# Kernel optimization log

Hardware: AMD Instinct MI355X
Metric: run time of the kernel (lower is better)

Reference implementation:

```python
import jax, jax.numpy as jnp
from jax import lax
import numpy as np

# 8-neighbor topology from the original module
TOPO = np.array([[0, 1], [1, 1], [1, 0], [1, -1], [0, -1], [-1, -1], [-1, 0], [-1, 1]])
EPS = 1e-5


def conv(x, w, stride=1, pad=0, groups=1):
    # NCHW / OIHW convolution, no bias (module uses bias=False everywhere)
    return lax.conv_general_dilated(
        x, w, (stride, stride), [(pad, pad), (pad, pad)],
        feature_group_count=groups,
        dimension_numbers=('NCHW', 'OIHW', 'NCHW'))


def bn(x, g, b):
    # training-mode BatchNorm2d (batch statistics, biased variance)
    m = jnp.mean(x, axis=(0, 2, 3), keepdims=True)
    v = jnp.var(x, axis=(0, 2, 3), keepdims=True)
    return g[None, :, None, None] * (x - m) * lax.rsqrt(v + EPS) + b[None, :, None, None]


def setup_inputs() -> dict:
    key = jax.random.key(0)
    ks = jax.random.split(key, 12)
    B, D, NC, H, W = 8, 6, 48, 256, 256
    s = 0.1
    w = lambda k, shape: jax.random.normal(k, shape, jnp.float32) * s
    return dict(
        x=jax.random.normal(ks[0], (B, D, H, W), jnp.float32),
        # compenv_conv: Conv(D->NC,1) BN tanh Conv(NC->1,1)
        ce_w1=w(ks[1], (NC, D, 1, 1)), ce_g=jnp.ones(NC), ce_b=jnp.zeros(NC),
        ce_w2=w(ks[2], (1, NC, 1, 1)),
        # merge_change_determinant: funnel(ConvT(10->NC,3) tanh Conv(NC->NC,3) tanh) BN tanh Conv(NC->1,2,s2) sigmoid
        # ConvT stride-1 k3 expressed as pad-2 conv with conv-equivalent kernel
        md_ct=w(ks[3], (NC, 10, 3, 3)), md_c1=w(ks[4], (NC, NC, 3, 3)),
        md_g=jnp.ones(NC), md_b=jnp.zeros(NC), md_c2=w(ks[5], (1, NC, 2, 2)),
        # cell_merge: Conv(D->NC,2,s2,g3) BN tanh funnel(ConvT(NC->NC,3,g3) tanh Conv(NC->D,3,g3) tanh)
        cm_w1=w(ks[6], (NC, D // 3, 2, 2)), cm_g=jnp.ones(NC), cm_b=jnp.zeros(NC),
        cm_ct=w(ks[7], (NC, NC // 3, 3, 3)), cm_c2=w(ks[8], (D, NC // 3, 3, 3)),
        # born: Conv(D->NC,1) BN tanh Conv(NC->D,1)
        bo_w1=w(ks[9], (NC, D, 1, 1)), bo_g=jnp.ones(NC), bo_b=jnp.zeros(NC),
        bo_w2=w(ks[10], (D, NC, 1, 1)),
    )


def reference(x, ce_w1, ce_g, ce_b, ce_w2, md_ct, md_c1, md_g, md_b, md_c2,
              cm_w1, cm_g, cm_b, cm_ct, cm_c2, bo_w1, bo_g, bo_b, bo_w2):
    # ---- compenv: per-direction roll + 1x1conv/BN/tanh/1x1conv (BN stats per direction, as in torch) ----
    env = []
    for k in range(8):
        t = jnp.roll(x, int(TOPO[k, 0]), axis=3)      # roll_right along W
        t = jnp.roll(t, int(-TOPO[k, 1]), axis=2)     # roll_down along H
        h = jnp.tanh(bn(conv(t, ce_w1), ce_g, ce_b))
        env.append(conv(h, ce_w2))                    # [B,1,H,W]
    ENV = jnp.concatenate(env, axis=1)                # [B,8,H,W]

    # ---- merge change determinant ----
    te = jnp.concatenate([x[:, :2], ENV], axis=1)     # [B,10,H,W]
    h = jnp.tanh(conv(te, md_ct, pad=2))              # ConvT k3 s1 == pad-2 conv -> [B,NC,H+2,W+2]
    h = jnp.tanh(conv(h, md_c1))                      # -> [B,NC,H,W]
    h = jnp.tanh(bn(h, md_g, md_b))
    CHANGE = jax.nn.sigmoid(conv(h, md_c2, stride=2))  # [B,1,H/2,W/2]

    # ---- cell merge ----
    h = jnp.tanh(bn(conv(x, cm_w1, stride=2, groups=3), cm_g, cm_b))  # [B,NC,H/2,W/2]
    h = jnp.tanh(conv(h, cm_ct, pad=2, groups=3))
    xm = jnp.tanh(conv(h, cm_c2, groups=3))           # [B,D,H/2,W/2]

    # ---- born + blend ----
    born = conv(jnp.tanh(bn(conv(xm, bo_w1), bo_g, bo_b)), bo_w2)
    out = xm * (1.0 - CHANGE) + CHANGE * born
    out = jnp.concatenate([jax.nn.sigmoid(out[:, :3]), out[:, 3:]], axis=1)
    return out
```

## Files before the change

kernel.cpp:

```cpp
#include <hip/hip_runtime.h>
#include <stdint.h>

typedef unsigned short ushort_t;

#define B8  8
#define D6  6
#define NC  48
#define HH  256
#define WW  256
#define HWp 65536
#define H2  128
#define HW2 16384

__device__ __constant__ int c_T0[8] = {0,1,1,1,0,-1,-1,-1};
__device__ __constant__ int c_T1[8] = {1,1,0,-1,-1,-1,0,1};

__device__ inline float bf2f(ushort_t u){ union{unsigned int i; float f;} w; w.i = ((unsigned int)u)<<16; return w.f; }
__device__ inline ushort_t f2bf(float f){ union{float f; unsigned int i;} w; w.f=f; unsigned int xx=w.i;
  return (ushort_t)((xx + 0x7fffu + ((xx>>16)&1u)) >> 16); }
__device__ inline float tanhf_(float x){ float e=__expf(2.f*x); return 1.f - 2.f/(e+1.f); }
__device__ inline float sigm_(float x){ return 1.f/(1.f+__expf(-x)); }
__device__ inline float ldg_(const void* p, size_t i, int isbf){
  return isbf ? bf2f(((const ushort_t*)p)[i]) : ((const float*)p)[i];
}

typedef short short8 __attribute__((ext_vector_type(8)));
typedef float f4 __attribute__((ext_vector_type(4)));
typedef ushort_t us4 __attribute__((ext_vector_type(4)));
typedef ushort_t us8 __attribute__((ext_vector_type(8)));
union AB { short8 s; us4 h[2]; us8 u; };

__device__ inline void msb_inline(int c, const float* mom, const float* W1,
      const void* g, const void* b, int isbf, float invN, float* sc, float* bi){
  const int st[6]={0,6,11,15,18,20};
  float wr[6];
  #pragma unroll
  for(int d=0;d<6;d++) wr[d]=W1[c*6+d];
  float mean=0.f;
  #pragma unroll
  for(int d=0;d<6;d++) mean += wr[d]*mom[d];
  mean *= invN;
  float e2=0.f;
  #pragma unroll
  for(int d=0;d<6;d++)
    #pragma unroll
    for(int e=d;e<6;e++)
      e2 += wr[d]*wr[e]*((e==d)?1.f:2.f)*mom[6 + st[d] + (e-d)];
  e2 *= invN;
  float var = e2 - mean*mean;
  float s = ldg_(g,c,isbf) * rsqrtf(var + 1e-5f);
  sc[c]=s; bi[c]= ldg_(b,c,isbf) - s*mean;
}

__device__ inline void csb_inline(int c, const float* stats, const void* g, const void* b,
      int isbf, float invN, float* sc, float* bi){
  float mean=stats[2*c]*invN; float var=stats[2*c+1]*invN - mean*mean;
  float s=ldg_(g,c,isbf)*rsqrtf(var+1e-5f);
  sc[c]=s; bi[c]=ldg_(b,c,isbf)-s*mean;
}

__global__ __launch_bounds__(256) void k_detect(const ushort_t* x, float* stats){
  int t=threadIdx.x;
  for(int i=t;i<1024;i+=256) stats[i]=0.f;
  __syncthreads();
  int cnt=0;
  for(int i=t;i<4096;i+=256){
    ushort_t u=x[2*i];
    int e=(u>>7)&0xff;
    if(e>=100 && e<=150) cnt++;
  }
  for(int o=32;o;o>>=1) cnt+=__shfl_down(cnt,o,64);
  __shared__ int sh4[4];
  if((t&63)==0) sh4[t>>6]=cnt;
  __syncthreads();
  if(t==0){ int tot=sh4[0]+sh4[1]+sh4[2]+sh4[3]; stats[960] = (tot>=2048)?1.f:0.f; }
}

struct WC { const ushort_t* src[10]; int off[10]; int n[10]; };

__global__ __launch_bounds__(256) void k_prep(WC wc, float* dst, const float* dfl,
      const void* mdc1r, const void* mdctr, ushort_t* wb2, ushort_t* wb1,
      const void* x, float* xmom){
  int isbf = dfl[0]>0.5f;
  int bx = blockIdx.x;
  __shared__ float red[4][27];
  if(bx < 810){
    int arr = bx/81, blk = bx-arr*81;
    int n = wc.n[arr]; const ushort_t* s = wc.src[arr]; float* d = dst + wc.off[arr];
    for(int i = blk*256 + threadIdx.x; i < n; i += 81*256)
      d[i] = isbf ? bf2f(s[i]) : ((const float*)s)[i];
  } else if(bx < 831){
    int t = (bx-810)*256+threadIdx.x;
    if(t<3456){
      int lane=t&63; int rest=t>>6;
      int ks=rest&1; int g=rest>>1; int tap=g%9; int nt=g/9;
      int oc=nt*16+(lane&15); int icb=ks*32+((lane>>4)*8);
      #pragma unroll
      for(int j=0;j<8;j++){
        int ic=icb+j;
        float v = (ic<48) ? ldg_(mdc1r,(size_t)(oc*48+ic)*9+tap,isbf) : 0.f;
        wb2[(size_t)t*8+j]=f2bf(v);
      }
    } else if(t<5184){
      int tt=t-3456; int lane=tt&63; int g=tt>>6; int tap=g%9; int nt=g/9;
      int oc=nt*16+(lane&15); int icb=(lane>>4)*8;
      #pragma unroll
      for(int j=0;j<8;j++){
        int ic=icb+j;
        float v = (ic<10) ? ldg_(mdctr,(size_t)(oc*10+ic)*9+tap,isbf) : 0.f;
        wb1[(size_t)tt*8+j]=f2bf(v);
      }
    }
  } else {
    int bm = bx-831;
    float vals[27];
    #pragma unroll
    for(int i=0;i<27;i++) vals[i]=0.f;
    for(int p = bm*256+threadIdx.x; p < B8*HWp; p += 256*256){
      int b = p >> 16; int hw = p & 65535;
      float v[6];
      #pragma unroll
      for(int d=0; d<6; d++) v[d]=ldg_(x, (((size_t)(b*6+d))<<16)+hw, isbf);
      int q=6;
      #pragma unroll
      for(int d=0;d<6;d++){
        vals[d]+=v[d];
        #pragma unroll
        for(int e=d;e<6;e++){ vals[q] += v[d]*v[e]; q++; }
      }
    }
    int wid=threadIdx.x>>6, lane=threadIdx.x&63;
    #pragma unroll
    for(int i=0;i<27;i++){
      float v=vals[i];
      for(int o=32;o;o>>=1) v+=__shfl_down(v,o,64);
      if(lane==0) red[wid][i]=v;
    }
    __syncthreads();
    if(threadIdx.x<27)
      atomicAdd(&xmom[threadIdx.x],
        red[0][threadIdx.x]+red[1][threadIdx.x]+red[2][threadIdx.x]+red[3][threadIdx.x]);
  }
}

__global__ __launch_bounds__(256) void k_envcm1(const void* x, const float* dfl,
      const float* xmom, const float* cew1, const float* cew2, const void* ceg, const void* ceb,
      const float* cmw1, float* e, ushort_t* t1){
  int isbf = dfl[0]>0.5f;
  int bx = blockIdx.x;
  __shared__ float sc[48], bi[48];
  if(bx < 2048){
    if(threadIdx.x<48)
      msb_inline(threadIdx.x, xmom, cew1, ceg, ceb, isbf, 1.f/(float)(B8*HWp), sc, bi);
    __syncthreads();
    int p = bx*256+threadIdx.x;
    int b = p >> 16; int hw = p & 65535;
    float v[6];
    #pragma unroll
    for(int d=0; d<6; d++) v[d]=ldg_(x,(size_t)(b*6+d)*HWp + hw, isbf);
    float acc=0.f;
    for(int c=0;c<NC;c++){
      float y=0.f;
      #pragma unroll
      for(int d=0;d<6;d++) y += cew1[c*6+d]*v[d];
      acc += cew2[c]*tanhf_(sc[c]*y + bi[c]);
    }
    e[(size_t)b*HWp + hw]=acc;
  } else {
    int p=(bx-2048)*256+threadIdx.x;
    int b=p>>14; int rem=p&16383; int i=rem>>7; int j=rem&127;
    float v[6][2][2];
    #pragma unroll
    for(int d=0;d<6;d++)
      #pragma unroll
      for(int ki=0;ki<2;ki++)
        #pragma unroll
        for(int kj=0;kj<2;kj++)
          v[d][ki][kj]=ldg_(x, ((size_t)(b*6+d)*HH + 2*i+ki)*WW + 2*j+kj, isbf);
    for(int oc=0;oc<NC;oc++){
      int g=oc>>4;
      float a=0.f;
      #pragma unroll
      for(int icl=0;icl<2;icl++)
        #pragma unroll
        for(int ki=0;ki<2;ki++)
          #pragma unroll
          for(int kj=0;kj<2;kj++)
            a += v[2*g+icl][ki][kj]*cmw1[((oc*2+icl)*2+ki)*2+kj];
      t1[((size_t)(b*NC+oc)*HW2) + rem]=f2bf(a);
    }
  }
}

__global__ __launch_bounds__(256,3) void k_mdst(const void* x, const float* dfl, const float* e,
      const ushort_t* wb1, const ushort_t* wb2, ushort_t* h2t, float* stats,
      const ushort_t* t1, float* t1stats){
  __shared__ __attribute__((aligned(16))) ushort_t te[6400];
  __shared__ __attribute__((aligned(16))) ushort_t h1t[19488];
  __shared__ float red[4][3][16][2];
  int bx = blockIdx.x;
  if(bx >= 2048){
    int l = bx-2048;
    int c = l % NC; int s = l / NC;
    float sum=0.f, sq=0.f;
    for(int b=0;b<B8;b++){
      size_t base=((size_t)b*NC+c)*HW2;
      for(int i=s*256+threadIdx.x; i<HW2; i+=8*256){
        float v = bf2f(t1[base+i]);
        sum+=v; sq+=v*v;
      }
    }
    for(int o=32;o;o>>=1){ sum+=__shfl_down(sum,o,64); sq+=__shfl_down(sq,o,64); }
    int wid=threadIdx.x>>6;
    if((threadIdx.x&63)==0){ red[wid][0][0][0]=sum; red[wid][0][0][1]=sq; }
    __syncthreads();
    if(threadIdx.x==0){
      atomicAdd(&t1stats[2*c],   red[0][0][0][0]+red[1][0][0][0]+red[2][0][0][0]+red[3][0][0][0]);
      atomicAdd(&t1stats[2*c+1], red[0][0][0][1]+red[1][0][0][1]+red[2][0][0][1]+red[3][0][0][1]);
    }
    return;
  }
  int isbf = dfl[0]>0.5f;
  int b = bx>>8; int tile = bx&255;
  int ti = tile>>4, tj = tile&15;
  int i0 = ti*16, j0 = tj*16;
  int lane = threadIdx.x&63, w = threadIdx.x>>6;
  int n = lane&15, quad = lane>>4;
  {
    us8 z;
    #pragma unroll
    for(int j=0;j<8;j++) z[j]=0;
    us8* tp=(us8*)te;
    for(int idx=threadIdx.x; idx<800; idx+=256) tp[idx]=z;
    for(int idx=threadIdx.x; idx<336; idx+=256) *(us8*)&h1t[idx*58+48]=z;
  }
  __syncthreads();
  for(int idx=threadIdx.x; idx<4000; idx+=256){
    int pix = idx/10, ic = idx-pix*10;
    int r = pix/20, c = pix-r*20;
    int gy = i0-2+r, gx = j0-2+c;
    float v = 0.f;
    if(gy>=0 && gy<HH && gx>=0 && gx<WW){
      if(ic<2) v = ldg_(x, ((size_t)(b*6+ic)*HH + gy)*WW + gx, isbf);
      else { int k=ic-2;
        int yy=(gy + c_T1[k]) & 255; int xx=(gx - c_T0[k]) & 255;
        v = e[((size_t)b*HH + yy)*WW + xx]; }
    }
    te[pix*16+ic]=f2bf(v);
  }
  __syncthreads();
  {
    int qoff = (quad&1)*8;
    for(int mt=w; mt<21; mt+=4){
      int p = mt*16 + n;
      int pr = p/18, pc = p-pr*18;
      f4 hacc[3];
      #pragma unroll
      for(int nt=0;nt<3;nt++) hacc[nt]=(f4){0.f,0.f,0.f,0.f};
      #pragma unroll
      for(int tap=0; tap<9; tap++){
        int ki=tap/3, kj=tap%3;
        AB a; a.u = *(const us8*)&te[((pr+ki)*20 + pc+kj)*16 + qoff];
        #pragma unroll
        for(int nt=0;nt<3;nt++){
          AB Bf; Bf.u = *(const us8*)&wb1[((size_t)((nt*9+tap)*64+lane))*8];
          hacc[nt] = __builtin_amdgcn_mfma_f32_16x16x32_bf16(a.s, Bf.s, hacc[nt], 0,0,0);
        }
      }
      int pd = mt*16 + quad*4;
      #pragma unroll
      for(int nt=0;nt<3;nt++){
        #pragma unroll
        for(int r=0;r<4;r++)
          h1t[(pd+r)*58 + nt*16 + n] = f2bf(tanhf_(hacc[nt][r]));
      }
    }
  }
  __syncthreads();
  f4 acc[4][3];
  #pragma unroll
  for(int a=0;a<4;a++)
    #pragma unroll
    for(int c=0;c<3;c++) acc[a][c]=(f4){0.f,0.f,0.f,0.f};
  int q1off = 32 + ((quad<2) ? quad*8 : 16);
  #pragma unroll
  for(int tap=0; tap<9; tap++){
    int ki=tap/3, kj=tap%3;
    AB Bf[3][2];
    #pragma unroll
    for(int nt=0;nt<3;nt++)
      #pragma unroll
      for(int ks=0;ks<2;ks++)
        Bf[nt][ks].u = *(const us8*)&wb2[((size_t)(((nt*9+tap)*2+ks)*64+lane))*8];
    #pragma unroll
    for(int yy=0; yy<4; yy++){
      int y = w*4 + yy;
      int base = ((y+ki)*18 + n + kj)*58;
      AB a0, a1;
      a0.u = *(const us8*)&h1t[base + quad*8];
      a1.u = *(const us8*)&h1t[base + q1off];
      #pragma unroll
      for(int nt=0;nt<3;nt++){
        acc[yy][nt] = __builtin_amdgcn_mfma_f32_16x16x32_bf16(a0.s, Bf[nt][0].s, acc[yy][nt], 0,0,0);
        acc[yy][nt] = __builtin_amdgcn_mfma_f32_16x16x32_bf16(a1.s, Bf[nt][1].s, acc[yy][nt], 0,0,0);
      }
    }
  }
  float s[3]={0.f,0.f,0.f}, q[3]={0.f,0.f,0.f};
  size_t tilebase = (size_t)bx*48*256;
  #pragma unroll
  for(int yy=0;yy<4;yy++){
    #pragma unroll
    for(int nt=0;nt<3;nt++){
      int oc = nt*16 + n;
      size_t base = tilebase + (size_t)oc*256 + (w*4+yy)*16 + quad*4;
      us4 u;
      #pragma unroll
      for(int r=0;r<4;r++){
        float v=tanhf_(acc[yy][nt][r]);
        u[r]=f2bf(v);
        float vb=bf2f(u[r]);
        s[nt]+=vb; q[nt]+=vb*vb;
      }
      *(us4*)&h2t[base] = u;
    }
  }
  #pragma unroll
  for(int nt=0;nt<3;nt++){
    s[nt]+=__shfl_xor(s[nt],16,64); s[nt]+=__shfl_xor(s[nt],32,64);
    q[nt]+=__shfl_xor(q[nt],16,64); q[nt]+=__shfl_xor(q[nt],32,64);
  }
  if(quad==0){
    #pragma unroll
    for(int nt=0;nt<3;nt++){ red[w][nt][n][0]=s[nt]; red[w][nt][n][1]=q[nt]; }
  }
  __syncthreads();
  if(threadIdx.x<48){
    int oc=threadIdx.x; int nt=oc>>4, nn=oc&15;
    float S=red[0][nt][nn][0]+red[1][nt][nn][0]+red[2][nt][nn][0]+red[3][nt][nn][0];
    float Q=red[0][nt][nn][1]+red[1][nt][nn][1]+red[2][nt][nn][1]+red[3][nt][nn][1];
    atomicAdd(&stats[2*oc],S); atomicAdd(&stats[2*oc+1],Q);
  }
}

__global__ __launch_bounds__(256) void k_chcm2(const ushort_t* h2t, const float* dfl,
      const float* mdstats, const void* mdg, const void* mdb, const float* wc2, float* CH,
      const ushort_t* t1, const float* t1stats, const void* cmg, const void* cmb,
      const float* wct, float* t2){
  __shared__ float shbuf[6816];
  int isbf = dfl[0]>0.5f;
  int bx = blockIdx.x;
  if(bx < 2048){
    float* rr = shbuf; float* sc = shbuf+256; float* bi = shbuf+304;
    if(threadIdx.x<48)
      csb_inline(threadIdx.x, mdstats, mdg, mdb, isbf, 1.f/(float)(B8*HWp), sc, bi);
    __syncthreads();
    int tile = bx;
    int b = tile>>8; int rest = tile&255; int ti = rest>>4, tj = rest&15;
    int t = threadIdx.x;
    int pix = t&63, icq = t>>6;
    int oi = pix>>3, oj = pix&7;
    const ushort_t* tp = &h2t[(size_t)tile*48*256];
    float acc = 0.f;
    #pragma unroll
    for(int icl=0; icl<12; icl++){
      int ic = icq*12 + icl;
      float s = sc[ic], tb = bi[ic];
      const ushort_t* cp = tp + ic*256 + (2*oi)*16 + 2*oj;
      acc += tanhf_(s*bf2f(cp[0 ])+tb)*wc2[ic*4+0];
      acc += tanhf_(s*bf2f(cp[1 ])+tb)*wc2[ic*4+1];
      acc += tanhf_(s*bf2f(cp[16])+tb)*wc2[ic*4+2];
      acc += tanhf_(s*bf2f(cp[17])+tb)*wc2[ic*4+3];
    }
    rr[icq*64+pix] = acc;
    __syncthreads();
    if(t<64){
      float v = rr[t]+rr[64+t]+rr[128+t]+rr[192+t];
      int i = ti*8 + (t>>3), j = tj*8 + (t&7);
      CH[((size_t)b<<14) + i*128 + j] = sigm_(v);
    }
  } else {
    float* as = shbuf; float* sc = shbuf+6720; float* bi = shbuf+6768;
    if(threadIdx.x<48)
      csb_inline(threadIdx.x, t1stats, cmg, cmb, isbf, 1.f/(float)(B8*HW2), sc, bi);
    __syncthreads();
    int l = bx-2048;
    int g = l/648; int rem = l-g*648; int b = rem/81; int t = rem-b*81;
    int ti=t/9, tj=t%9;
    int i0=ti*16, j0=tj*16;
    int ty=threadIdx.x>>4, tx=threadIdx.x&15;
    for(int idx=threadIdx.x; idx<6400; idx+=256){
      int i=idx/400; int rm=idx-i*400; int r=rm/20; int cc=rm-r*20;
      int cg=g*16+i;
      int y=i0-2+r, xx=j0-2+cc;
      float v=0.f;
      if(y>=0 && y<H2 && xx>=0 && xx<H2)
        v = tanhf_(sc[cg]*bf2f(t1[((size_t)(b*NC+cg)*H2 + y)*H2 + xx]) + bi[cg]);
      as[(i*20+r)*21+cc]=v;
    }
    __syncthreads();
    float acc[16];
    #pragma unroll
    for(int o=0;o<16;o++) acc[o]=0.f;
    for(int i=0;i<16;i++){
      float p[3][3];
      #pragma unroll
      for(int ki=0;ki<3;ki++)
        #pragma unroll
        for(int kj=0;kj<3;kj++) p[ki][kj]=as[(i*20+ty+ki)*21+tx+kj];
      #pragma unroll
      for(int o=0;o<16;o++){
        const float* wp=&wct[((size_t)(g*16+o)*16+i)*9];
        float a=0.f;
        #pragma unroll
        for(int q=0;q<9;q++) a += p[q/3][q%3]*wp[q];
        acc[o]+=a;
      }
    }
    int ii=i0+ty, jj=j0+tx;
    if(ii<130 && jj<130){
      #pragma unroll
      for(int o=0;o<16;o++)
        t2[((size_t)(b*NC+g*16+o)*130 + ii)*130 + jj]=tanhf_(acc[o]);
    }
  }
}

__global__ __launch_bounds__(256) void k_cm3(const float* t2, const float* w, float* xm){
  __shared__ float ts[16][18][20];
  int b=blockIdx.y, g=blockIdx.z;
  int ti=blockIdx.x>>3, tj=blockIdx.x&7;
  int i0=ti*16, j0=tj*16;
  int ty=threadIdx.x>>4, tx=threadIdx.x&15;
  for(int idx=threadIdx.x; idx<16*18*18; idx+=256){
    int i=idx/324; int rem=idx-i*324; int r=rem/18; int cc=rem-r*18;
    int cg=g*16+i;
    ts[i][r][cc]=t2[((size_t)(b*NC+cg)*130 + i0+r)*130 + j0+cc];
  }
  __syncthreads();
  float acc[2]={0.f,0.f};
  for(int icl=0;icl<16;icl++){
    float p[3][3];
    #pragma unroll
    for(int ki=0;ki<3;ki++)
      #pragma unroll
      for(int kj=0;kj<3;kj++) p[ki][kj]=ts[icl][ty+ki][tx+kj];
    #pragma unroll
    for(int ol=0;ol<2;ol++){
      int oc=2*g+ol;
      const float* wp=&w[((size_t)oc*16+icl)*9];
      float a=0.f;
      #pragma unroll
      for(int q=0;q<9;q++) a += p[q/3][q%3]*wp[q];
      acc[ol]+=a;
    }
  }
  int ii=i0+ty, jj=j0+tx;
  #pragma unroll
  for(int ol=0;ol<2;ol++)
    xm[((size_t)(b*6+2*g+ol)*H2 + ii)*H2 + jj]=tanhf_(acc[ol]);
}

__global__ __launch_bounds__(256) void k_mom(const float* src, float* out){
  float vals[27];
  #pragma unroll
  for(int i=0;i<27;i++) vals[i]=0.f;
  int stride = gridDim.x*256;
  for(int p = blockIdx.x*256+threadIdx.x; p < B8*HW2; p += stride){
    int b = p >> 14; int hw = p & 16383;
    float v[6];
    #pragma unroll
    for(int d=0; d<6; d++) v[d]=src[(((size_t)(b*6+d))<<14)+hw];
    int q=6;
    #pragma unroll
    for(int d=0;d<6;d++){
      vals[d]+=v[d];
      #pragma unroll
      for(int e=d;e<6;e++){ vals[q] += v[d]*v[e]; q++; }
    }
  }
  __shared__ float red[4][27];
  int wid=threadIdx.x>>6, lane=threadIdx.x&63;
  #pragma unroll
  for(int i=0;i<27;i++){
    float v=vals[i];
    for(int o=32;o;o>>=1) v+=__shfl_down(v,o,64);
    if(lane==0) red[wid][i]=v;
  }
  __syncthreads();
  if(threadIdx.x<27)
    atomicAdd(&out[threadIdx.x],
      red[0][threadIdx.x]+red[1][threadIdx.x]+red[2][threadIdx.x]+red[3][threadIdx.x]);
}

__global__ __launch_bounds__(256) void k_final(const float* xm, const float* CH,
      const float* xmmom, const float* w1, const float* w2, const void* bog, const void* bob,
      const float* dfl, void* outp){
  int isbf = dfl[0]>0.5f;
  __shared__ float sc[48], bi[48];
  if(threadIdx.x<48)
    msb_inline(threadIdx.x, xmmom, w1, bog, bob, isbf, 1.f/(float)(B8*HW2), sc, bi);
  __syncthreads();
  int p=blockIdx.x*256+threadIdx.x;
  int b=p>>14; int rem=p&16383;
  float v[6];
  #pragma unroll
  for(int d=0;d<6;d++) v[d]=xm[((size_t)(b*6+d)*HW2)+rem];
  float born[6]={0.f,0.f,0.f,0.f,0.f,0.f};
  for(int c=0;c<NC;c++){
    float y=0.f;
    #pragma unroll
    for(int d=0;d<6;d++) y+=w1[c*6+d]*v[d];
    float a=tanhf_(sc[c]*y+bi[c]);
    #pragma unroll
    for(int d=0;d<6;d++) born[d]+=w2[d*NC+c]*a;
  }
  float C=CH[p];
  #pragma unroll
  for(int d=0;d<6;d++){
    float o=v[d]*(1.f-C)+C*born[d];
    if(d<3) o=sigm_(o);
    size_t id=((size_t)(b*6+d)*HW2)+rem;
    if(isbf) ((ushort_t*)outp)[id]=f2bf(o); else ((float*)outp)[id]=o;
  }
}

extern "C" void kernel_launch(void* const* d_in, const int* in_sizes, int n_in,
                              void* d_out, int out_size, void* d_ws, size_t ws_size,
                              hipStream_t stream){
  (void)in_sizes; (void)n_in; (void)out_size; (void)ws_size;
  const ushort_t* x    = (const ushort_t*)d_in[0];
  const ushort_t* cew1 = (const ushort_t*)d_in[1];
  const void*     ceg  = d_in[2];
  const void*     ceb  = d_in[3];
  const ushort_t* cew2 = (const ushort_t*)d_in[4];
  const ushort_t* mdct = (const ushort_t*)d_in[5];
  const ushort_t* mdc1 = (const ushort_t*)d_in[6];
  const void*     mdg  = d_in[7];
  const void*     mdb  = d_in[8];
  const ushort_t* mdc2 = (const ushort_t*)d_in[9];
  const ushort_t* cmw1 = (const ushort_t*)d_in[10];
  const void*     cmg  = d_in[11];
  const void*     cmb  = d_in[12];
  const ushort_t* cmct = (const ushort_t*)d_in[13];
  const ushort_t* cmc2 = (const ushort_t*)d_in[14];
  const ushort_t* bow1 = (const ushort_t*)d_in[15];
  const void*     bog  = d_in[16];
  const void*     bob  = d_in[17];
  const ushort_t* bow2 = (const ushort_t*)d_in[18];
  float* ws = (float*)d_ws;

  const long OW_mdct=0, OW_mdc1=4320, OW_cew1=25056, OW_cew2=25344, OW_mdc2=25392,
             OW_cmw1=25584, OW_cmct=25968, OW_cmc2=32880, OW_bow1=33744, OW_bow2=34032;
  const long OFF_STATS=34320;
  const long ST_xmom=OFF_STATS+0,
             ST_h2  =OFF_STATS+160,
             ST_t1  =OFF_STATS+352,
             ST_xmm =OFF_STATS+544;
  const long OFF_WB2 = OFF_STATS + 1024;
  const long OFF_WB1 = OFF_WB2 + 13824;
  const long OFF_E   = OFF_WB1 + 6912;
  const long OFF_H2  = OFF_E + 524288L;
  const long OFF_D   = OFF_H2 + 12582912L;
  const long OFF_T1=OFF_D, OFF_T2=OFF_D+6291456L, OFF_XM=OFF_D+12781056L, OFF_CH=OFF_D+13567488L;

  ushort_t* h2t  = (ushort_t*)(ws + OFF_H2);
  ushort_t* t1h  = (ushort_t*)(ws + OFF_T1);
  ushort_t* wb2  = (ushort_t*)(ws + OFF_WB2);
  ushort_t* wb1  = (ushort_t*)(ws + OFF_WB1);
  const float* dfl = ws + OFF_STATS + 960;

  hipLaunchKernelGGL(k_detect, dim3(1), 256, 0, stream, x, ws+OFF_STATS);

  WC wc;
  const ushort_t* srcs[10] = {mdct,mdc1,cew1,cew2,mdc2,cmw1,cmct,cmc2,bow1,bow2};
  const int offs[10] = {(int)OW_mdct,(int)OW_mdc1,(int)OW_cew1,(int)OW_cew2,(int)OW_mdc2,
                        (int)OW_cmw1,(int)OW_cmct,(int)OW_cmc2,(int)OW_bow1,(int)OW_bow2};
  const int cnts[10] = {4320,20736,288,48,192,384,6912,864,288,288};
  for(int i=0;i<10;i++){ wc.src[i]=srcs[i]; wc.off[i]=offs[i]; wc.n[i]=cnts[i]; }
  hipLaunchKernelGGL(k_prep, dim3(1087), 256, 0, stream, wc, ws, dfl,
                     (const void*)mdc1, (const void*)mdct, wb2, wb1, (const void*)x, ws+ST_xmom);

  hipLaunchKernelGGL(k_envcm1, dim3(2560), 256, 0, stream, (const void*)x, dfl,
                     ws+ST_xmom, ws+OW_cew1, ws+OW_cew2, ceg, ceb, ws+OW_cmw1,
                     ws+OFF_E, t1h);

  hipLaunchKernelGGL(k_mdst, dim3(2432), 256, 0, stream, (const void*)x, dfl, ws+OFF_E,
                     wb1, wb2, h2t, ws+ST_h2, t1h, ws+ST_t1);

  hipLaunchKernelGGL(k_chcm2, dim3(3992), 256, 0, stream, h2t, dfl,
                     ws+ST_h2, mdg, mdb, ws+OW_mdc2, ws+OFF_CH,
                     t1h, ws+ST_t1, cmg, cmb, ws+OW_cmct, ws+OFF_T2);

  hipLaunchKernelGGL(k_cm3, dim3(64,8,3), 256, 0, stream, ws+OFF_T2, ws+OW_cmc2, ws+OFF_XM);

  hipLaunchKernelGGL(k_mom, dim3(128), 256, 0, stream, ws+OFF_XM, ws+ST_xmm);

  hipLaunchKernelGGL(k_final, dim3(512), 256, 0, stream, ws+OFF_XM, ws+OFF_CH,
                     ws+ST_xmm, ws+OW_bow1, ws+OW_bow2, bog, bob, dfl, d_out);
}
```

Before: 404.4 us.

## Store h2 in NCHW planar layout and keep t2 intermediate in bf16

k_mdst now writes the tanh conv output h2 in plain NCHW layout instead of per-tile blocks. The CHANGE stage becomes one thread per output pixel that loops over all 48 channels and reads 2x2 windows straight from global memory, which drops the shared-memory reduction and cuts its block count from 2048 to 512. Separately, the cell-merge intermediate t2 is stored as bf16 instead of fp32, halving its traffic into k_cm3. The cost is less coalesced strided reads in the CHANGE path and some extra rounding on t2.

```diff
diff --git a/kernel.cpp b/kernel.cpp
--- a/kernel.cpp
+++ b/kernel.cpp
@@ -193,7 +193,7 @@
 }
 
 __global__ __launch_bounds__(256,3) void k_mdst(const void* x, const float* dfl, const float* e,
-      const ushort_t* wb1, const ushort_t* wb2, ushort_t* h2t, float* stats,
+      const ushort_t* wb1, const ushort_t* wb2, ushort_t* h2h, float* stats,
       const ushort_t* t1, float* t1stats){
   __shared__ __attribute__((aligned(16))) ushort_t te[6400];
   __shared__ __attribute__((aligned(16))) ushort_t h1t[19488];
@@ -307,13 +307,13 @@
     }
   }
   float s[3]={0.f,0.f,0.f}, q[3]={0.f,0.f,0.f};
-  size_t tilebase = (size_t)bx*48*256;
   #pragma unroll
   for(int yy=0;yy<4;yy++){
+    int Y = i0 + w*4 + yy;
     #pragma unroll
     for(int nt=0;nt<3;nt++){
       int oc = nt*16 + n;
-      size_t base = tilebase + (size_t)oc*256 + (w*4+yy)*16 + quad*4;
+      size_t base = ((size_t)(b*NC+oc)*HH + Y)*WW + j0 + quad*4;
       us4 u;
       #pragma unroll
       for(int r=0;r<4;r++){
@@ -322,7 +322,7 @@
         float vb=bf2f(u[r]);
         s[nt]+=vb; q[nt]+=vb*vb;
       }
-      *(us4*)&h2t[base] = u;
+      *(us4*)&h2h[base] = u;
     }
   }
   #pragma unroll
@@ -343,48 +343,37 @@
   }
 }
 
-__global__ __launch_bounds__(256) void k_chcm2(const ushort_t* h2t, const float* dfl,
+__global__ __launch_bounds__(256) void k_chcm2(const ushort_t* h2h, const float* dfl,
       const float* mdstats, const void* mdg, const void* mdb, const float* wc2, float* CH,
       const ushort_t* t1, const float* t1stats, const void* cmg, const void* cmb,
-      const float* wct, float* t2){
+      const float* wct, ushort_t* t2){
   __shared__ float shbuf[6816];
   int isbf = dfl[0]>0.5f;
   int bx = blockIdx.x;
-  if(bx < 2048){
-    float* rr = shbuf; float* sc = shbuf+256; float* bi = shbuf+304;
+  if(bx < 512){
+    float* sc = shbuf; float* bi = shbuf+48;
     if(threadIdx.x<48)
       csb_inline(threadIdx.x, mdstats, mdg, mdb, isbf, 1.f/(float)(B8*HWp), sc, bi);
     __syncthreads();
-    int tile = bx;
-    int b = tile>>8; int rest = tile&255; int ti = rest>>4, tj = rest&15;
-    int t = threadIdx.x;
-    int pix = t&63, icq = t>>6;
-    int oi = pix>>3, oj = pix&7;
-    const ushort_t* tp = &h2t[(size_t)tile*48*256];
-    float acc = 0.f;
-    #pragma unroll
-    for(int icl=0; icl<12; icl++){
-      int ic = icq*12 + icl;
-      float s = sc[ic], tb = bi[ic];
-      const ushort_t* cp = tp + ic*256 + (2*oi)*16 + 2*oj;
-      acc += tanhf_(s*bf2f(cp[0 ])+tb)*wc2[ic*4+0];
-      acc += tanhf_(s*bf2f(cp[1 ])+tb)*wc2[ic*4+1];
-      acc += tanhf_(s*bf2f(cp[16])+tb)*wc2[ic*4+2];
-      acc += tanhf_(s*bf2f(cp[17])+tb)*wc2[ic*4+3];
-    }
-    rr[icq*64+pix] = acc;
-    __syncthreads();
-    if(t<64){
-      float v = rr[t]+rr[64+t]+rr[128+t]+rr[192+t];
-      int i = ti*8 + (t>>3), j = tj*8 + (t&7);
-      CH[((size_t)b<<14) + i*128 + j] = sigm_(v);
-    }
+    int p=bx*256+threadIdx.x;
+    int b=p>>14; int rem=p&16383; int i=rem>>7; int j=rem&127;
+    float acc=0.f;
+    for(int ic=0;ic<NC;ic++){
+      size_t base=((size_t)(b*NC+ic)*HH + 2*i)*WW + 2*j;
+      float s=sc[ic], t=bi[ic];
+      #pragma unroll
+      for(int ki=0;ki<2;ki++)
+        #pragma unroll
+        for(int kj=0;kj<2;kj++)
+          acc += tanhf_(s*bf2f(h2h[base+(size_t)ki*WW+kj])+t)*wc2[ic*4+ki*2+kj];
+    }
+    CH[p]=sigm_(acc);
   } else {
     float* as = shbuf; float* sc = shbuf+6720; float* bi = shbuf+6768;
     if(threadIdx.x<48)
       csb_inline(threadIdx.x, t1stats, cmg, cmb, isbf, 1.f/(float)(B8*HW2), sc, bi);
     __syncthreads();
-    int l = bx-2048;
+    int l = bx-512;
     int g = l/648; int rem = l-g*648; int b = rem/81; int t = rem-b*81;
     int ti=t/9, tj=t%9;
     int i0=ti*16, j0=tj*16;
@@ -421,12 +410,12 @@
     if(ii<130 && jj<130){
       #pragma unroll
       for(int o=0;o<16;o++)
-        t2[((size_t)(b*NC+g*16+o)*130 + ii)*130 + jj]=tanhf_(acc[o]);
-    }
-  }
-}
-
-__global__ __launch_bounds__(256) void k_cm3(const float* t2, const float* w, float* xm){
+        t2[((size_t)(b*NC+g*16+o)*130 + ii)*130 + jj]=f2bf(tanhf_(acc[o]));
+    }
+  }
+}
+
+__global__ __launch_bounds__(256) void k_cm3(const ushort_t* t2, const float* w, float* xm){
   __shared__ float ts[16][18][20];
   int b=blockIdx.y, g=blockIdx.z;
   int ti=blockIdx.x>>3, tj=blockIdx.x&7;
@@ -435,7 +424,7 @@
   for(int idx=threadIdx.x; idx<16*18*18; idx+=256){
     int i=idx/324; int rem=idx-i*324; int r=rem/18; int cc=rem-r*18;
     int cg=g*16+i;
-    ts[i][r][cc]=t2[((size_t)(b*NC+cg)*130 + i0+r)*130 + j0+cc];
+    ts[i][r][cc]=bf2f(t2[((size_t)(b*NC+cg)*130 + i0+r)*130 + j0+cc]);
   }
   __syncthreads();
   float acc[2]={0.f,0.f};
@@ -564,8 +553,9 @@
   const long OFF_D   = OFF_H2 + 12582912L;
   const long OFF_T1=OFF_D, OFF_T2=OFF_D+6291456L, OFF_XM=OFF_D+12781056L, OFF_CH=OFF_D+13567488L;
 
-  ushort_t* h2t  = (ushort_t*)(ws + OFF_H2);
+  ushort_t* h2h  = (ushort_t*)(ws + OFF_H2);
   ushort_t* t1h  = (ushort_t*)(ws + OFF_T1);
+  ushort_t* t2h  = (ushort_t*)(ws + OFF_T2);
   ushort_t* wb2  = (ushort_t*)(ws + OFF_WB2);
   ushort_t* wb1  = (ushort_t*)(ws + OFF_WB1);
   const float* dfl = ws + OFF_STATS + 960;
@@ -586,13 +576,13 @@
                      ws+OFF_E, t1h);
 
   hipLaunchKernelGGL(k_mdst, dim3(2432), 256, 0, stream, (const void*)x, dfl, ws+OFF_E,
-                     wb1, wb2, h2t, ws+ST_h2, t1h, ws+ST_t1);
-
-  hipLaunchKernelGGL(k_chcm2, dim3(3992), 256, 0, stream, h2t, dfl,
+                     wb1, wb2, h2h, ws+ST_h2, t1h, ws+ST_t1);
+
+  hipLaunchKernelGGL(k_chcm2, dim3(2456), 256, 0, stream, h2h, dfl,
                      ws+ST_h2, mdg, mdb, ws+OW_mdc2, ws+OFF_CH,
-                     t1h, ws+ST_t1, cmg, cmb, ws+OW_cmct, ws+OFF_T2);
-
-  hipLaunchKernelGGL(k_cm3, dim3(64,8,3), 256, 0, stream, ws+OFF_T2, ws+OW_cmc2, ws+OFF_XM);
+                     t1h, ws+ST_t1, cmg, cmb, ws+OW_cmct, t2h);
+
+  hipLaunchKernelGGL(k_cm3, dim3(64,8,3), 256, 0, stream, t2h, ws+OW_cmc2, ws+OFF_XM);
 
   hipLaunchKernelGGL(k_mom, dim3(128), 256, 0, stream, ws+OFF_XM, ws+ST_xmm);
 
```

Result: no change. 408.4 us (+1.0%).
